# Performance work log

Hardware: AMD Instinct MI355X
Metric: run time of the kernel (lower is better)

## Reference

```python
import jax, jax.numpy as jnp
import numpy as np

BLOCK_SIZE = 32
TAU = 0.1
E2M1_VALUES = np.array([0.0, 0.5, 1.0, 1.5, 2.0, 3.0, 4.0, 6.0], dtype=np.float32)
E2M1_BOUNDS = np.array([0.25, 0.75, 1.25, 1.75, 2.5, 3.5, 5.0], dtype=np.float32)


def setup_inputs() -> dict:
    key = jax.random.key(0)
    x = jax.random.normal(key, (2048, 4096), dtype=jnp.float32)
    return {
        "x": x,
        "delta_raw": jnp.zeros((), dtype=jnp.float32),
        "bounds_base": jnp.asarray(E2M1_BOUNDS),
        "values_table": jnp.asarray(E2M1_VALUES),
    }


def reference(x, delta_raw, bounds_base, values_table):
    orig_shape = x.shape
    bs = BLOCK_SIZE
    xb = x.reshape(-1, bs)  # [n_blocks, bs]
    # per-block e8m0 power-of-two scale from amax
    amax = jnp.max(jnp.abs(xb), axis=-1, keepdims=True)
    descale = amax / 6.0
    e8m0_scale = jnp.ceil(jnp.maximum(jnp.log2(descale), -127.0))
    scale_factor = jnp.exp2(e8m0_scale)
    x_scaled = (xb / scale_factor).reshape(orig_shape)
    # perturbed decision bounds
    shifted_bounds = bounds_base + 0.5 * jnp.tanh(delta_raw)  # [7]
    x_abs = jnp.abs(x_scaled)
    # hard ordinal bucketize: count bounds exceeded -> code in [0,7]
    ord_hard = jnp.sum(x_abs[..., None] > shifted_bounds, axis=-1)  # int32
    sign_bit = (x_scaled < 0).astype(jnp.uint8)
    codes = (sign_bit << 3) | ord_hard.astype(jnp.uint8)
    # soft ordinal weights via sigmoid at each boundary
    p = jax.nn.sigmoid((x_abs[..., None] - shifted_bounds) / TAU)  # [..., 7]
    w0 = 1.0 - p[..., 0]
    mids = p[..., :-1] - p[..., 1:]
    w_last = p[..., -1]
    weights = jnp.concatenate([w0[..., None], mids, w_last[..., None]], axis=-1)  # [..., 8]
    weights = jnp.clip(weights, 0.0)
    weights = weights / (jnp.sum(weights, axis=-1, keepdims=True) + 1e-8)
    abs_soft = jnp.sum(weights * values_table, axis=-1)
    abs_hard = values_table[ord_hard]
    # straight-through: hard value forward, soft gradient
    abs_mix = abs_soft + jax.lax.stop_gradient(abs_hard - abs_soft)
    y_scaled = jnp.where(x_scaled >= 0, abs_mix, -abs_mix)
    y = (y_scaled.reshape(-1, bs) * scale_factor).reshape(orig_shape)
    scales = (e8m0_scale + 127.0).astype(jnp.uint8)[:, 0].reshape(
        *orig_shape[:-1], orig_shape[-1] // bs
    )
    return (y, codes, scales, shifted_bounds, weights)
```

## Files before the change

kernel.cpp:

```cpp
#include <hip/hip_runtime.h>

#define BLK 256
#define EPT 2
#define ELEMS (BLK * EPT)
#define WFLOATS (ELEMS * 8)

__device__ __forceinline__ int swz_q(int q) { return q ^ ((q >> 4) & 7); }
__device__ __forceinline__ int swz(int p)  { return (swz_q(p >> 2) << 2) | (p & 3); }

__global__ __launch_bounds__(BLK, 8) void fp4_kernel(
    const float* __restrict__ x,
    const float* __restrict__ delta_raw,
    const float* __restrict__ bounds_base,
    const float* __restrict__ values_table,
    float* __restrict__ out, long long N)
{
    const int tid = threadIdx.x;
    const long long base = (long long)blockIdx.x * ELEMS;
    const long long g0 = base + 2 * tid;

    __shared__ float s_vals[8];
    __shared__ __align__(16) float s_w[WFLOATS];

    if (tid < 8) s_vals[tid] = values_table[tid];

    float ht = 0.5f * tanhf(delta_raw[0]);
    ht = __int_as_float(__builtin_amdgcn_readfirstlane(__float_as_int(ht)));
    const float C = 14.426950408889634f;
    float sb[7], cb[7];
#pragma unroll
    for (int j = 0; j < 7; ++j) { sb[j] = bounds_base[j] + ht; cb[j] = sb[j] * C; }
    float vt[8];
#pragma unroll
    for (int k = 0; k < 8; ++k) vt[k] = values_table[k];

    __syncthreads();

    const float2 xv = *reinterpret_cast<const float2*>(x + g0);
    const float xe[EPT] = {xv.x, xv.y};

    float a = fmaxf(fabsf(xe[0]), fabsf(xe[1]));
    a = fmaxf(a, __shfl_xor(a, 1));
    a = fmaxf(a, __shfl_xor(a, 2));
    a = fmaxf(a, __shfl_xor(a, 4));
    a = fmaxf(a, __shfl_xor(a, 8));

    const float descale = a / 6.0f;
    const float e = ceilf(fmaxf(log2f(descale), -127.0f));
    const int ie = (int)e;
    const float inv_scale = __int_as_float((127 - ie) << 23);
    const float scale = (ie == -127) ? __int_as_float(0x00400000)
                                     : __int_as_float((ie + 127) << 23);

    float ys[EPT], cd[EPT];

#pragma unroll
    for (int i = 0; i < EPT; ++i) {
        const float xs = xe[i] * inv_scale;
        const float xa = fabsf(xs);

        int ord = 0;
#pragma unroll
        for (int j = 0; j < 7; ++j) ord += (xa > sb[j]) ? 1 : 0;

        const float xac = xa * C;
        float p[7];
#pragma unroll
        for (int j = 0; j < 7; ++j) {
            const float ex = exp2f(cb[j] - xac);
            p[j] = __builtin_amdgcn_rcpf(1.0f + ex);
        }

        float w[8];
        w[0] = 1.0f - p[0];
#pragma unroll
        for (int j = 1; j < 7; ++j) w[j] = p[j - 1] - p[j];
        w[7] = p[6];

        float sum = 0.0f;
#pragma unroll
        for (int k = 0; k < 8; ++k) { w[k] = fmaxf(w[k], 0.0f); sum += w[k]; }
        const float inv = __builtin_amdgcn_rcpf(sum + 1e-8f);

        float abs_soft = 0.0f;
#pragma unroll
        for (int k = 0; k < 8; ++k) { w[k] *= inv; abs_soft += w[k] * vt[k]; }

        const float abs_hard = s_vals[ord];
        const float abs_mix = abs_soft + (abs_hard - abs_soft);
        ys[i] = ((xs >= 0.0f) ? abs_mix : -abs_mix) * scale;
        cd[i] = (float)(((xs < 0.0f) ? 8 : 0) | ord);

        const int el = 2 * tid + i;
        s_w[swz(((el << 3) - 1) & (WFLOATS - 1))] = w[0];
        *reinterpret_cast<float4*>(&s_w[swz_q(el << 1) << 2]) =
            make_float4(w[1], w[2], w[3], w[4]);
        const int qb = swz_q((el << 1) | 1) << 2;
        *reinterpret_cast<float2*>(&s_w[qb]) = make_float2(w[5], w[6]);
        s_w[qb + 2] = w[7];
    }

    *reinterpret_cast<float2*>(out + g0)     = make_float2(ys[0], ys[1]);
    *reinterpret_cast<float2*>(out + N + g0) = make_float2(cd[0], cd[1]);
    if ((tid & 15) == 0) out[2 * N + (g0 >> 5)] = e + 127.0f;
    if (blockIdx.x == 0 && tid < 7) {
        float v = sb[0];
#pragma unroll
        for (int j = 1; j < 7; ++j) v = (tid == j) ? sb[j] : v;
        out[2 * N + (N >> 5) + tid] = v;
    }

    __syncthreads();

    const long long S = 2 * N + (N >> 5) + 7 + (long long)blockIdx.x * WFLOATS;
#pragma unroll
    for (int k = 0; k < 4; ++k) {
        const int q = tid + (k << 8);
        const float4 v = *reinterpret_cast<const float4*>(&s_w[swz_q(q) << 2]);
        if (q != 1023) {
            *reinterpret_cast<float4*>(out + (S + 1 + 4 * (long long)q)) = v;
        } else {
            out[S + 4093] = v.x;
            out[S + 4094] = v.y;
            out[S + 4095] = v.z;
            out[S]        = v.w;
        }
    }
}

extern "C" void kernel_launch(void* const* d_in, const int* in_sizes, int n_in,
                              void* d_out, int out_size, void* d_ws, size_t ws_size,
                              hipStream_t stream) {
    const float* x      = (const float*)d_in[0];
    const float* delta  = (const float*)d_in[1];
    const float* bounds = (const float*)d_in[2];
    const float* vals   = (const float*)d_in[3];
    float* out = (float*)d_out;
    const long long N = (long long)in_sizes[0];
    const int nblocks = (int)(N / ELEMS);
    fp4_kernel<<<nblocks, BLK, 0, stream>>>(x, delta, bounds, vals, out, N);
}
```

Measured before the change: 359.8 us.

## Write weights directly from registers with lane shuffles instead of LDS staging

The weights output is no longer staged through a swizzled shared-memory buffer with block-wide barriers. Each thread writes its 16 weights directly as float4 stores shifted by one float, taking the neighbour lane's first weight through a shuffle. Wavefront-boundary lanes fall back to scalar stores. The hard-value lookup also moves from shared memory to a register select chain, which removes LDS use and both __syncthreads, at the cost of global stores whose alignment and coalescing pattern differs.

```diff
diff --git a/kernel.cpp b/kernel.cpp
--- a/kernel.cpp
+++ b/kernel.cpp
@@ -3,12 +3,8 @@
 #define BLK 256
 #define EPT 2
 #define ELEMS (BLK * EPT)
-#define WFLOATS (ELEMS * 8)
 
-__device__ __forceinline__ int swz_q(int q) { return q ^ ((q >> 4) & 7); }
-__device__ __forceinline__ int swz(int p)  { return (swz_q(p >> 2) << 2) | (p & 3); }
-
-__global__ __launch_bounds__(BLK, 8) void fp4_kernel(
+__global__ __launch_bounds__(BLK) void fp4_kernel(
     const float* __restrict__ x,
     const float* __restrict__ delta_raw,
     const float* __restrict__ bounds_base,
@@ -19,11 +15,6 @@
     const long long base = (long long)blockIdx.x * ELEMS;
     const long long g0 = base + 2 * tid;
 
-    __shared__ float s_vals[8];
-    __shared__ __align__(16) float s_w[WFLOATS];
-
-    if (tid < 8) s_vals[tid] = values_table[tid];
-
     float ht = 0.5f * tanhf(delta_raw[0]);
     ht = __int_as_float(__builtin_amdgcn_readfirstlane(__float_as_int(ht)));
     const float C = 14.426950408889634f;
@@ -33,8 +24,6 @@
     float vt[8];
 #pragma unroll
     for (int k = 0; k < 8; ++k) vt[k] = values_table[k];
-
-    __syncthreads();
 
     const float2 xv = *reinterpret_cast<const float2*>(x + g0);
     const float xe[EPT] = {xv.x, xv.y};
@@ -53,9 +42,11 @@
                                      : __int_as_float((ie + 127) << 23);
 
     float ys[EPT], cd[EPT];
+    float wa[8], wb[8];
 
 #pragma unroll
     for (int i = 0; i < EPT; ++i) {
+        float* w = (i == 0) ? wa : wb;
         const float xs = xe[i] * inv_scale;
         const float xa = fabsf(xs);
 
@@ -71,7 +62,6 @@
             p[j] = __builtin_amdgcn_rcpf(1.0f + ex);
         }
 
-        float w[8];
         w[0] = 1.0f - p[0];
 #pragma unroll
         for (int j = 1; j < 7; ++j) w[j] = p[j - 1] - p[j];
@@ -86,18 +76,13 @@
 #pragma unroll
         for (int k = 0; k < 8; ++k) { w[k] *= inv; abs_soft += w[k] * vt[k]; }
 
-        const float abs_hard = s_vals[ord];
+        float abs_hard = vt[0];
+#pragma unroll
+        for (int k = 1; k < 8; ++k) abs_hard = (ord == k) ? vt[k] : abs_hard;
+
         const float abs_mix = abs_soft + (abs_hard - abs_soft);
         ys[i] = ((xs >= 0.0f) ? abs_mix : -abs_mix) * scale;
         cd[i] = (float)(((xs < 0.0f) ? 8 : 0) | ord);
-
-        const int el = 2 * tid + i;
-        s_w[swz(((el << 3) - 1) & (WFLOATS - 1))] = w[0];
-        *reinterpret_cast<float4*>(&s_w[swz_q(el << 1) << 2]) =
-            make_float4(w[1], w[2], w[3], w[4]);
-        const int qb = swz_q((el << 1) | 1) << 2;
-        *reinterpret_cast<float2*>(&s_w[qb]) = make_float2(w[5], w[6]);
-        s_w[qb + 2] = w[7];
     }
 
     *reinterpret_cast<float2*>(out + g0)     = make_float2(ys[0], ys[1]);
@@ -110,22 +95,23 @@
         out[2 * N + (N >> 5) + tid] = v;
     }
 
-    __syncthreads();
+    const long long S = 2 * N + (N >> 5) + 7 + (long long)blockIdx.x * (ELEMS * 8);
+    const long long tb = S + 16 * (long long)tid;
+    const float nw0 = __shfl_down(wa[0], 1);
+    const int lane = tid & 63;
 
-    const long long S = 2 * N + (N >> 5) + 7 + (long long)blockIdx.x * WFLOATS;
-#pragma unroll
-    for (int k = 0; k < 4; ++k) {
-        const int q = tid + (k << 8);
-        const float4 v = *reinterpret_cast<const float4*>(&s_w[swz_q(q) << 2]);
-        if (q != 1023) {
-            *reinterpret_cast<float4*>(out + (S + 1 + 4 * (long long)q)) = v;
-        } else {
-            out[S + 4093] = v.x;
-            out[S + 4094] = v.y;
-            out[S + 4095] = v.z;
-            out[S]        = v.w;
-        }
+    *reinterpret_cast<float4*>(out + tb + 1) = make_float4(wa[1], wa[2], wa[3], wa[4]);
+    *reinterpret_cast<float4*>(out + tb + 5) = make_float4(wa[5], wa[6], wa[7], wb[0]);
+    *reinterpret_cast<float4*>(out + tb + 9) = make_float4(wb[1], wb[2], wb[3], wb[4]);
+    if (lane != 63) {
+        *reinterpret_cast<float4*>(out + tb + 13) =
+            make_float4(wb[5], wb[6], wb[7], nw0);
+    } else {
+        out[tb + 13] = wb[5];
+        out[tb + 14] = wb[6];
+        out[tb + 15] = wb[7];
     }
+    if (lane == 0) out[tb] = wa[0];
 }
 
 extern "C" void kernel_launch(void* const* d_in, const int* in_sizes, int n_in,
```

Measured after the change: 401.9 us. +11.7%, slower.
